# Kernel optimization log

Measured on AMD Instinct MI355X. Metric: run time of the kernel, lower is better.

## Reference

```python
import jax, jax.numpy as jnp
import numpy as np

N_HEAD = 16
G_HEADS = 2
D_HEAD = 64
D_MODEL = 1024
HEAD_RATIO = N_HEAD // G_HEADS  # 8
QK_DIM = G_HEADS * D_HEAD       # 128
SCALE = 1.0 / D_HEAD ** 0.5
LN_EPS = 1e-5


def _rel_shift(x):
    # x: [qlen, rlen, B, n] -- Transformer-XL relative shift
    q, r = x.shape[0], x.shape[1]
    x_pad = jnp.pad(x, ((0, 0), (1, 0), (0, 0), (0, 0)))      # [q, r+1, B, n]
    x_pad = x_pad.reshape(r + 1, q, *x.shape[2:])[1:]          # drop first row
    return x_pad.reshape(q, r, *x.shape[2:])


def setup_inputs() -> dict:
    key = jax.random.key(0)
    ks = jax.random.split(key, 9)
    qlen, bsz, levels = 1024, 4, 3
    w = jax.random.normal(ks[0], (qlen, bsz, D_MODEL), jnp.float32)
    r = jax.random.normal(ks[1], (qlen, D_MODEL), jnp.float32)
    r_w_bias = jax.random.normal(ks[2], (G_HEADS, D_HEAD), jnp.float32) * 0.02
    r_r_bias = jax.random.normal(ks[3], (G_HEADS, D_HEAD), jnp.float32) * 0.02
    masks = jax.random.uniform(ks[4], (qlen, qlen, levels), jnp.float32)
    W_qkv = jax.random.normal(ks[5], (2 * QK_DIM + N_HEAD * D_HEAD, D_MODEL), jnp.float32) * 0.02
    W_r = jax.random.normal(ks[6], (QK_DIM, D_MODEL), jnp.float32) * 0.02
    mask_proj = jnp.ones((levels, N_HEAD), jnp.float32)
    W_o = jax.random.normal(ks[7], (D_MODEL, N_HEAD * D_HEAD), jnp.float32) * 0.02
    ln_gamma = jnp.ones((D_MODEL,), jnp.float32)
    ln_beta = jnp.zeros((D_MODEL,), jnp.float32)
    return dict(w=w, r=r, r_w_bias=r_w_bias, r_r_bias=r_r_bias, masks=masks,
                W_qkv=W_qkv, W_r=W_r, mask_proj=mask_proj, W_o=W_o,
                ln_gamma=ln_gamma, ln_beta=ln_beta)


def reference(w, r, r_w_bias, r_r_bias, masks, W_qkv, W_r, mask_proj, W_o, ln_gamma, ln_beta):
    qlen, bsz, _ = w.shape
    rlen = r.shape[0]
    N = qlen  # no mems: klen == qlen == rlen

    w_heads = w @ W_qkv.T                                   # [q, B, 1280]
    r_head_k = (r @ W_r.T).reshape(rlen, G_HEADS, D_HEAD)   # [r, gH, d]
    w_head_q = w_heads[..., :QK_DIM].reshape(qlen, bsz, G_HEADS, D_HEAD)
    w_head_k = w_heads[..., QK_DIM:2 * QK_DIM].reshape(qlen, bsz, G_HEADS, D_HEAD)
    w_head_v = w_heads[..., 2 * QK_DIM:].reshape(qlen, bsz, N_HEAD, D_HEAD)

    AC = jnp.einsum('ibnd,jbnd->ijbn', w_head_q + r_w_bias, w_head_k)
    BD = jnp.einsum('ibnd,jnd->ijbn', w_head_q + r_r_bias, r_head_k)
    BD = _rel_shift(BD)
    attn_score = (AC + BD) * SCALE                           # [N, N, B, gH]

    # per-head mask mixing ('full' projection)
    attn = jnp.transpose(attn_score, (2, 3, 0, 1))           # [B, gH, N, N]
    mw = (masks @ mask_proj).reshape(N, N, G_HEADS, HEAD_RATIO)
    mw = jnp.transpose(mw, (2, 0, 1, 3))                     # [gH, N, N, hr]
    attn = attn[..., None] * mw[None]                        # [B, gH, N, N, hr]
    attn = jnp.transpose(attn, (0, 1, 4, 2, 3)).reshape(bsz, N_HEAD, N, N)
    attn_score = jnp.transpose(attn, (2, 3, 0, 1))           # [N, N, B, H]

    attn_prob = jax.nn.softmax(attn_score, axis=1)
    attn_vec = jnp.einsum('ijbn,jbnd->ibnd', attn_prob, w_head_v)
    attn_vec = attn_vec.reshape(qlen, bsz, N_HEAD * D_HEAD)
    attn_out = attn_vec @ W_o.T                              # [q, B, d_model]

    # post-LN residual
    x = w + attn_out
    mu = jnp.mean(x, axis=-1, keepdims=True)
    var = jnp.mean((x - mu) ** 2, axis=-1, keepdims=True)
    return (x - mu) * jax.lax.rsqrt(var + LN_EPS) * ln_gamma + ln_beta
```

## Files before the change

kernel.cpp:

```cpp
#include <hip/hip_runtime.h>
#include <cstddef>
#include <cstdint>

#define QLEN   1024
#define SCALE  0.125f
#define LN_EPS 1e-5f
#define DMODEL 1024

typedef __bf16 bf16x8 __attribute__((ext_vector_type(8)));
typedef __bf16 bf16x4 __attribute__((ext_vector_type(4)));
typedef float  f32x4  __attribute__((ext_vector_type(4)));

__device__ __forceinline__ void load16_lds(const void* g, void* l) {
  __builtin_amdgcn_global_load_lds(
      (const __attribute__((address_space(1))) unsigned int*)g,
      (__attribute__((address_space(3))) unsigned int*)l, 16, 0, 0);
}

__device__ __forceinline__ void bar_lds() {
  asm volatile("s_waitcnt lgkmcnt(0)" ::: "memory");
  __builtin_amdgcn_s_barrier();
  asm volatile("" ::: "memory");
}

__global__ __launch_bounds__(256) void cast_all(
    const float* __restrict__ w, __bf16* __restrict__ w_bf,
    const float* __restrict__ Wqkv, __bf16* __restrict__ Wqkv_bf,
    const float* __restrict__ r, __bf16* __restrict__ r_bf,
    const float* __restrict__ Wr, __bf16* __restrict__ Wr_bf,
    const float* __restrict__ Wo, __bf16* __restrict__ Wo_bf)
{
  int blk = blockIdx.x;
  const float* in; __bf16* out;
  if (blk < 2048)      { in = w;    out = w_bf;    }
  else if (blk < 2688) { blk -= 2048; in = Wqkv; out = Wqkv_bf; }
  else if (blk < 3200) { blk -= 2688; in = r;    out = r_bf;    }
  else if (blk < 3264) { blk -= 3200; in = Wr;   out = Wr_bf;   }
  else                 { blk -= 3264; in = Wo;   out = Wo_bf;   }
  const size_t i = ((size_t)blk * 256 + threadIdx.x) * 8;
  const float4 a = *(const float4*)&in[i];
  const float4 b = *(const float4*)&in[i + 4];
  bf16x8 o;
  o[0] = (__bf16)a.x; o[1] = (__bf16)a.y; o[2] = (__bf16)a.z; o[3] = (__bf16)a.w;
  o[4] = (__bf16)b.x; o[5] = (__bf16)b.y; o[6] = (__bf16)b.z; o[7] = (__bf16)b.w;
  *(bf16x8*)&out[i] = o;
}

__global__ __launch_bounds__(256) void gemm_proj(
    const __bf16* __restrict__ w_bf, const __bf16* __restrict__ Wqkv_bf,
    const __bf16* __restrict__ r_bf, const __bf16* __restrict__ Wr_bf,
    const float* __restrict__ rwb, const float* __restrict__ rrb,
    __bf16* __restrict__ Qw, __bf16* __restrict__ Qr,
    __bf16* __restrict__ Kb, __bf16* __restrict__ Vt,
    __bf16* __restrict__ Rb)
{
  __shared__ __bf16 Asl[128 * 32];
  __shared__ __bf16 Bsl[64 * 32];
  const int blk = blockIdx.x;
  const bool isR = blk >= 640;
  const __bf16 *A, *B;
  int m0, n0;
  if (!isR) { A = w_bf; B = Wqkv_bf; n0 = (blk % 20) * 64; m0 = (blk / 20) * 128; }
  else      { const int k = blk - 640; A = r_bf; B = Wr_bf;
              n0 = (k % 2) * 64; m0 = (k / 2) * 128; }

  const int tid = threadIdx.x, lane = tid & 63, wv = tid >> 6;
  const int lr = lane & 15, kq = lane >> 4;
  const int srow  = wv * 16 + (lane >> 2);
  const int sslot = lane & 3;
  const int sg0 = (sslot - ((srow >> 1) & 3)) & 3;
  const int sg1 = (sslot - (((srow + 64) >> 1) & 3)) & 3;
  const __bf16* Ag = A + (size_t)(m0 + srow) * 1024;
  const __bf16* Bg = B + (size_t)(n0 + srow) * 1024;
  __bf16* Al = &Asl[srow * 32 + sslot * 8];
  __bf16* Bl = &Bsl[srow * 32 + sslot * 8];

  f32x4 acc[2][4];
#pragma unroll
  for (int mt = 0; mt < 2; ++mt)
#pragma unroll
    for (int nt = 0; nt < 4; ++nt)
      acc[mt][nt] = (f32x4){0.f, 0.f, 0.f, 0.f};

  for (int k0 = 0; k0 < 1024; k0 += 32) {
    load16_lds(Ag + k0 + sg0 * 8, Al);
    load16_lds(Ag + (size_t)64 * 1024 + k0 + sg1 * 8, Al + 64 * 32);
    load16_lds(Bg + k0 + sg0 * 8, Bl);
    __syncthreads();
    bf16x8 af[2], bfr[4];
#pragma unroll
    for (int mt = 0; mt < 2; ++mt) {
      const int row = wv * 32 + mt * 16 + lr;
      af[mt] = *(const bf16x8*)&Asl[row * 32 + ((kq + (row >> 1)) & 3) * 8];
    }
#pragma unroll
    for (int nt = 0; nt < 4; ++nt) {
      const int row = nt * 16 + lr;
      bfr[nt] = *(const bf16x8*)&Bsl[row * 32 + ((kq + (row >> 1)) & 3) * 8];
    }
#pragma unroll
    for (int mt = 0; mt < 2; ++mt)
#pragma unroll
      for (int nt = 0; nt < 4; ++nt)
        acc[mt][nt] = __builtin_amdgcn_mfma_f32_16x16x32_bf16(
            af[mt], bfr[nt], acc[mt][nt], 0, 0, 0);
    __syncthreads();
  }

#pragma unroll
  for (int mt = 0; mt < 2; ++mt) {
    const int row0 = m0 + wv * 32 + mt * 16 + kq * 4;
#pragma unroll
    for (int nt = 0; nt < 4; ++nt) {
      const int gcol = n0 + nt * 16 + lr;
      const f32x4 c = acc[mt][nt];
      if (isR) {
        const int g = gcol >> 6, d = gcol & 63;
#pragma unroll
        for (int reg = 0; reg < 4; ++reg)
          Rb[(size_t)g * 65536 + (size_t)(row0 + reg) * 64 + d] = (__bf16)c[reg];
      } else if (gcol < 128) {
        const int g = gcol >> 6, d = gcol & 63;
        const float bw = rwb[gcol], br = rrb[gcol];
#pragma unroll
        for (int reg = 0; reg < 4; ++reg) {
          const int row = row0 + reg, i = row >> 2, b = row & 3;
          const size_t o = (size_t)(b * 2 + g) * 65536 + (size_t)i * 64 + d;
          Qw[o] = (__bf16)(c[reg] + bw);
          Qr[o] = (__bf16)(c[reg] + br);
        }
      } else if (gcol < 256) {
        const int lc = gcol - 128, g = lc >> 6, d = lc & 63;
#pragma unroll
        for (int reg = 0; reg < 4; ++reg) {
          const int row = row0 + reg, i = row >> 2, b = row & 3;
          Kb[(size_t)(b * 2 + g) * 65536 + (size_t)i * 64 + d] = (__bf16)c[reg];
        }
      } else {
        const int lc = gcol - 256, h = lc >> 6, d = lc & 63;
#pragma unroll
        for (int reg = 0; reg < 4; ++reg) {
          const int row = row0 + reg, i = row >> 2, b = row & 3;
          Vt[((size_t)((b * 16 + h) * 64 + d)) * 1024 + i] = (__bf16)c[reg];
        }
      }
    }
  }
}

__global__ __launch_bounds__(256) void gemm_wo(
    const __bf16* __restrict__ A, const __bf16* __restrict__ B,
    float* __restrict__ C)
{
  __shared__ __bf16 Asl[128 * 32];
  __shared__ __bf16 Bsl[64 * 32];
  const int m0 = blockIdx.y * 128, n0 = blockIdx.x * 64;
  const int tid = threadIdx.x, lane = tid & 63, wv = tid >> 6;
  const int lr = lane & 15, kq = lane >> 4;
  const int srow  = wv * 16 + (lane >> 2);
  const int sslot = lane & 3;
  const int sg0 = (sslot - ((srow >> 1) & 3)) & 3;
  const int sg1 = (sslot - (((srow + 64) >> 1) & 3)) & 3;
  const __bf16* Ag = A + (size_t)(m0 + srow) * 1024;
  const __bf16* Bg = B + (size_t)(n0 + srow) * 1024;
  __bf16* Al = &Asl[srow * 32 + sslot * 8];
  __bf16* Bl = &Bsl[srow * 32 + sslot * 8];

  f32x4 acc[2][4];
#pragma unroll
  for (int mt = 0; mt < 2; ++mt)
#pragma unroll
    for (int nt = 0; nt < 4; ++nt)
      acc[mt][nt] = (f32x4){0.f, 0.f, 0.f, 0.f};

  for (int k0 = 0; k0 < 1024; k0 += 32) {
    load16_lds(Ag + k0 + sg0 * 8, Al);
    load16_lds(Ag + (size_t)64 * 1024 + k0 + sg1 * 8, Al + 64 * 32);
    load16_lds(Bg + k0 + sg0 * 8, Bl);
    __syncthreads();
    bf16x8 af[2], bfr[4];
#pragma unroll
    for (int mt = 0; mt < 2; ++mt) {
      const int row = wv * 32 + mt * 16 + lr;
      af[mt] = *(const bf16x8*)&Asl[row * 32 + ((kq + (row >> 1)) & 3) * 8];
    }
#pragma unroll
    for (int nt = 0; nt < 4; ++nt) {
      const int row = nt * 16 + lr;
      bfr[nt] = *(const bf16x8*)&Bsl[row * 32 + ((kq + (row >> 1)) & 3) * 8];
    }
#pragma unroll
    for (int mt = 0; mt < 2; ++mt)
#pragma unroll
      for (int nt = 0; nt < 4; ++nt)
        acc[mt][nt] = __builtin_amdgcn_mfma_f32_16x16x32_bf16(
            af[mt], bfr[nt], acc[mt][nt], 0, 0, 0);
    __syncthreads();
  }

#pragma unroll
  for (int mt = 0; mt < 2; ++mt) {
    const int row0 = m0 + wv * 32 + mt * 16 + kq * 4;
#pragma unroll
    for (int nt = 0; nt < 4; ++nt) {
      const int col = n0 + nt * 16 + lr;
      const f32x4 c = acc[mt][nt];
#pragma unroll
      for (int reg = 0; reg < 4; ++reg)
        C[(size_t)(row0 + reg) * 1024 + col] = c[reg];
    }
  }
}

__global__ __launch_bounds__(256) void gemm64_bf16(
    const __bf16* __restrict__ Qw, const __bf16* __restrict__ Qr,
    const __bf16* __restrict__ Kb, const __bf16* __restrict__ Rb,
    __bf16* __restrict__ AC, __bf16* __restrict__ BDo)
{
  __shared__ __bf16 Asl[128 * 64];
  __shared__ __bf16 Bsl[128 * 64];
  const int tid = threadIdx.x, lane = tid & 63, wv = tid >> 6;
  const int which = blockIdx.z & 1, bat = blockIdx.z >> 1;
  const int m0 = blockIdx.y * 128, n0 = blockIdx.x * 128;
  const __bf16* Ap = (which ? Qr : Qw) + (size_t)bat * 65536;
  const __bf16* Bp = which ? (Rb + (size_t)(bat & 1) * 65536)
                           : (Kb + (size_t)bat * 65536);
  __bf16* Cp = (which ? BDo : AC) + (size_t)bat * 1048576;

#pragma unroll
  for (int p = 0; p < 4; ++p) {
    const int row = wv * 32 + p * 8 + (lane >> 3);
    const int s = lane & 7;
    const int gc = (s - (row & 7)) & 7;
    load16_lds(Ap + (size_t)(m0 + row) * 64 + gc * 8, &Asl[row * 64 + s * 8]);
    load16_lds(Bp + (size_t)(n0 + row) * 64 + gc * 8, &Bsl[row * 64 + s * 8]);
  }
  __syncthreads();

  const int lr = lane & 15, kq = lane >> 4;
  const int wm = (wv >> 1) * 64, wn = (wv & 1) * 64;
  f32x4 acc[4][4];
#pragma unroll
  for (int mt = 0; mt < 4; ++mt)
#pragma unroll
    for (int nt = 0; nt < 4; ++nt)
      acc[mt][nt] = (f32x4){0.f, 0.f, 0.f, 0.f};

#pragma unroll
  for (int ks = 0; ks < 2; ++ks) {
    const int c = ks * 4 + kq;
    bf16x8 af[4], bfr[4];
#pragma unroll
    for (int mt = 0; mt < 4; ++mt) {
      const int row = wm + mt * 16 + lr;
      af[mt] = *(const bf16x8*)&Asl[row * 64 + ((c + (row & 7)) & 7) * 8];
    }
#pragma unroll
    for (int nt = 0; nt < 4; ++nt) {
      const int row = wn + nt * 16 + lr;
      bfr[nt] = *(const bf16x8*)&Bsl[row * 64 + ((c + (row & 7)) & 7) * 8];
    }
#pragma unroll
    for (int mt = 0; mt < 4; ++mt)
#pragma unroll
      for (int nt = 0; nt < 4; ++nt)
        acc[mt][nt] = __builtin_amdgcn_mfma_f32_16x16x32_bf16(
            af[mt], bfr[nt], acc[mt][nt], 0, 0, 0);
  }

#pragma unroll
  for (int mt = 0; mt < 4; ++mt) {
    const int row0 = m0 + wm + mt * 16 + kq * 4;
#pragma unroll
    for (int nt = 0; nt < 4; ++nt) {
      const int col = n0 + wn + nt * 16 + lr;
      const f32x4 cc = acc[mt][nt];
#pragma unroll
      for (int reg = 0; reg < 4; ++reg)
        Cp[(size_t)(row0 + reg) * 1024 + col] = (__bf16)cc[reg];
    }
  }
}

__global__ __launch_bounds__(256) void prep2(
    const __bf16* __restrict__ AC, const __bf16* __restrict__ BDm,
    __bf16* __restrict__ Tg,
    const float* __restrict__ masks, const float* __restrict__ mproj,
    __bf16* __restrict__ Mh)
{
  const int tid = threadIdx.x;
  if (blockIdx.x < 2048) {
    const int blk = blockIdx.x;
    const size_t bg = blk >> 8;
    const int i = (blk & 255) * 4 + (tid >> 6);
    const int lane = tid & 63;
    const __bf16* ACr = AC + bg * 1048576 + (size_t)i * 1024;
    const __bf16* BDb = BDm + bg * 1048576;
    __bf16* Tr = Tg + bg * 1048576 + (size_t)i * 1024;
#pragma unroll
    for (int c2 = 0; c2 < 4; ++c2) {
      const int j0 = c2 * 256 + lane * 4;
      const bf16x4 ac4 = *(const bf16x4*)&ACr[j0];
      bf16x4 o;
#pragma unroll
      for (int k = 0; k < 4; ++k) {
        const int j = j0 + k;
        float bd;
        if (j <= i)          bd = (float)BDb[(size_t)i * 1024 + (j + QLEN - 1 - i)];
        else if (j == i + 1) bd = 0.f;
        else                 bd = (float)BDb[(size_t)(i + 1) * 1024 + (j - i - 2)];
        o[k] = (__bf16)(((float)ac4[k] + bd) * SCALE);
      }
      *(bf16x4*)&Tr[j0] = o;
    }
  } else {
    const int blk = blockIdx.x - 2048;
    const size_t ij0 = ((size_t)blk * 256 + tid) * 4;
    const float4 a = *(const float4*)&masks[ij0 * 3];
    const float4 b = *(const float4*)&masks[ij0 * 3 + 4];
    const float4 c = *(const float4*)&masks[ij0 * 3 + 8];
    const float m0[4] = {a.x, a.w, b.z, c.y};
    const float m1[4] = {a.y, b.x, b.w, c.z};
    const float m2[4] = {a.z, b.y, c.x, c.w};
#pragma unroll
    for (int h = 0; h < 16; ++h) {
      const float p0 = mproj[h], p1 = mproj[16 + h], p2 = mproj[32 + h];
      bf16x4 o;
#pragma unroll
      for (int k = 0; k < 4; ++k)
        o[k] = (__bf16)(m0[k] * p0 + m1[k] * p1 + m2[k] * p2);
      *(bf16x4*)&Mh[(size_t)h * 1048576 + ij0] = o;
    }
  }
}

__global__ __launch_bounds__(256, 4) void attn8(
    const __bf16* __restrict__ Tg, const __bf16* __restrict__ Mh,
    const __bf16* __restrict__ Vt, __bf16* __restrict__ av)
{
  __shared__ __bf16 P[2][32 * 256];
  __shared__ float rinvS[32];
  const int tid = threadIdx.x;
  const int i0 = blockIdx.x * 32;
  const int h = blockIdx.y, b = blockIdx.z;
  const int g = h >> 3;
  const size_t bg = (size_t)(b * 2 + g);
  const int r = tid >> 3, li = tid & 7;
  const __bf16* Trow = Tg + bg * 1048576 + (size_t)(i0 + r) * 1024 + li * 8;
  const __bf16* Mrow = Mh + (size_t)h * 1048576 + (size_t)(i0 + r) * 1024 + li * 8;

  const int lane = tid & 63, wv = tid >> 6;
  const int m = lane & 15, kq = lane >> 4;
  const __bf16* vbase = Vt + ((size_t)((b * 16 + h) * 64 + wv * 16 + m)) * 1024 + kq * 8;

  float sum = 0.f;
  f32x4 acc[2][2];
#pragma unroll
  for (int mt = 0; mt < 2; ++mt)
#pragma unroll
    for (int u = 0; u < 2; ++u)
      acc[mt][u] = (f32x4){0.f, 0.f, 0.f, 0.f};

  bf16x8 t[4], mk[4], v[8];
#pragma unroll
  for (int q = 0; q < 4; ++q) {
    t[q]  = *(const bf16x8*)&Trow[q * 64];
    mk[q] = *(const bf16x8*)&Mrow[q * 64];
  }

  for (int ch = 0; ch < 4; ++ch) {
    const int cb = ch & 1;
#pragma unroll
    for (int ks = 0; ks < 8; ++ks)
      v[ks] = *(const bf16x8*)&vbase[(ch * 8 + ks) * 32];
#pragma unroll
    for (int q = 0; q < 4; ++q) {
      bf16x8 p8;
      float s0 = 0.f;
#pragma unroll
      for (int k = 0; k < 8; ++k) {
        const float e = __expf((float)t[q][k] * (float)mk[q][k]);
        s0 += e;
        p8[k] = (__bf16)e;
      }
      sum += s0;
      const int slot = (q * 8 + li) ^ (r & 7);
      *(bf16x8*)&P[cb][r * 256 + slot * 8] = p8;
    }
    if (ch < 3) {
#pragma unroll
      for (int q = 0; q < 4; ++q) {
        t[q]  = *(const bf16x8*)&Trow[(ch + 1) * 256 + q * 64];
        mk[q] = *(const bf16x8*)&Mrow[(ch + 1) * 256 + q * 64];
      }
    }
    bar_lds();
#pragma unroll
    for (int ks = 0; ks < 8; ++ks) {
      const int c = ks * 4 + kq;
#pragma unroll
      for (int mt = 0; mt < 2; ++mt) {
        const int R = mt * 16 + m;
        const bf16x8 a = *(const bf16x8*)&P[cb][R * 256 + ((c ^ (R & 7)) << 3)];
        acc[mt][ks & 1] = __builtin_amdgcn_mfma_f32_16x16x32_bf16(
            a, v[ks], acc[mt][ks & 1], 0, 0, 0);
      }
    }
  }

  sum += __shfl_xor(sum, 1);
  sum += __shfl_xor(sum, 2);
  sum += __shfl_xor(sum, 4);
  if (li == 0) rinvS[r] = 1.f / sum;
  __syncthreads();

#pragma unroll
  for (int mt = 0; mt < 2; ++mt) {
    const f32x4 accf = acc[mt][0] + acc[mt][1];
#pragma unroll
    for (int reg = 0; reg < 4; ++reg) {
      const int row = mt * 16 + kq * 4 + reg;
      av[((size_t)(i0 + row) * 4 + b) * 1024 + h * 64 + wv * 16 + m] =
          (__bf16)(accf[reg] * rinvS[row]);
    }
  }
}

__global__ __launch_bounds__(256) void ln_kernel(
    const float* __restrict__ w, const float* __restrict__ ao,
    const float* __restrict__ gamma, const float* __restrict__ beta,
    float* __restrict__ out)
{
  const int tid = threadIdx.x;
  const size_t base = (size_t)blockIdx.x * DMODEL;
  __shared__ float red[256];
  float x[4];
  float s = 0.f;
#pragma unroll
  for (int p = 0; p < 4; ++p) {
    const int c = tid + p * 256;
    x[p] = w[base + c] + ao[base + c];
    s += x[p];
  }
  red[tid] = s; __syncthreads();
  for (int off = 128; off > 0; off >>= 1) {
    if (tid < off) red[tid] += red[tid + off];
    __syncthreads();
  }
  const float mu = red[0] * (1.f / DMODEL);
  __syncthreads();
  float s2 = 0.f;
#pragma unroll
  for (int p = 0; p < 4; ++p) { const float t = x[p] - mu; s2 += t * t; }
  red[tid] = s2; __syncthreads();
  for (int off = 128; off > 0; off >>= 1) {
    if (tid < off) red[tid] += red[tid + off];
    __syncthreads();
  }
  const float rs = rsqrtf(red[0] * (1.f / DMODEL) + LN_EPS);
#pragma unroll
  for (int p = 0; p < 4; ++p) {
    const int c = tid + p * 256;
    out[base + c] = (x[p] - mu) * rs * gamma[c] + beta[c];
  }
}

extern "C" void kernel_launch(void* const* d_in, const int* in_sizes, int n_in,
                              void* d_out, int out_size, void* d_ws, size_t ws_size,
                              hipStream_t stream)
{
  const float* w     = (const float*)d_in[0];
  const float* r     = (const float*)d_in[1];
  const float* rwb   = (const float*)d_in[2];
  const float* rrb   = (const float*)d_in[3];
  const float* masks = (const float*)d_in[4];
  const float* Wqkv  = (const float*)d_in[5];
  const float* Wr    = (const float*)d_in[6];
  const float* mproj = (const float*)d_in[7];
  const float* Wo    = (const float*)d_in[8];
  const float* gam   = (const float*)d_in[9];
  const float* bet   = (const float*)d_in[10];
  float* out = (float*)d_out;

  float* ws = (float*)d_ws;
  __bf16* w_bf    = (__bf16*)(ws);
  __bf16* Wqkv_bf = (__bf16*)(ws + 2097152);
  __bf16* r_bf    = (__bf16*)(ws + 2752512);
  __bf16* Wr_bf   = (__bf16*)(ws + 3276800);
  __bf16* Qw      = (__bf16*)(ws + 3342336);
  __bf16* Qr      = (__bf16*)(ws + 3604480);
  __bf16* Kb      = (__bf16*)(ws + 3866624);
  __bf16* Rb      = (__bf16*)(ws + 4128768);
  __bf16* Mh      = (__bf16*)(ws);
  __bf16* AC_bf   = (__bf16*)(ws + 8388608);
  float*  ao      = ws + 8388608;
  __bf16* BD_bf   = (__bf16*)(ws + 12582912);
  __bf16* Tg      = (__bf16*)(ws + 16777216);
  __bf16* Vt      = (__bf16*)(ws + 20971520);
  __bf16* av_bf   = (__bf16*)(ws + 23068672);
  __bf16* Wo_bf   = (__bf16*)(ws + 25165824);

  cast_all<<<3776, 256, 0, stream>>>(w, w_bf, Wqkv, Wqkv_bf, r, r_bf,
                                     Wr, Wr_bf, Wo, Wo_bf);
  gemm_proj<<<656, 256, 0, stream>>>(
      w_bf, Wqkv_bf, r_bf, Wr_bf, rwb, rrb, Qw, Qr, Kb, Vt, Rb);
  gemm64_bf16<<<dim3(8, 8, 16), 256, 0, stream>>>(Qw, Qr, Kb, Rb, AC_bf, BD_bf);
  prep2<<<3072, 256, 0, stream>>>(AC_bf, BD_bf, Tg, masks, mproj, Mh);
  attn8<<<dim3(32, 16, 4), 256, 0, stream>>>(Tg, Mh, Vt, av_bf);
  gemm_wo<<<dim3(16, 32), 256, 0, stream>>>(av_bf, Wo_bf, ao);
  ln_kernel<<<4096, 256, 0, stream>>>(w, ao, gam, bet, out);
}
```

Before: 237.1 us.

## Fuse rel-shift into BD GEMM store, merge score add into attention, enlarge GEMM tiles

The BD GEMM now writes its output directly in rel-shifted layout, and the attention kernel adds AC and shifted BD and applies the scale itself. This removes the prep2 pass that materialised the combined score tensor, leaving prep_mask to do only the mask projection. The projection and output GEMMs move from 128x64 to 128x128 tiles with a 2x2 wave layout, so each block reuses more data but there are fewer blocks and more registers per thread. The layer norm switches to float4 loads and wave-shuffle reductions. Attention now reads two score tensors instead of one, and the shifted store in the GEMM epilogue is scattered.

```diff
diff --git a/kernel.cpp b/kernel.cpp
--- a/kernel.cpp
+++ b/kernel.cpp
@@ -55,19 +55,18 @@
     __bf16* __restrict__ Rb)
 {
   __shared__ __bf16 Asl[128 * 32];
-  __shared__ __bf16 Bsl[64 * 32];
+  __shared__ __bf16 Bsl[128 * 32];
   const int blk = blockIdx.x;
-  const bool isR = blk >= 640;
+  const bool isR = blk >= 320;
   const __bf16 *A, *B;
   int m0, n0;
-  if (!isR) { A = w_bf; B = Wqkv_bf; n0 = (blk % 20) * 64; m0 = (blk / 20) * 128; }
-  else      { const int k = blk - 640; A = r_bf; B = Wr_bf;
-              n0 = (k % 2) * 64; m0 = (k / 2) * 128; }
+  if (!isR) { A = w_bf; B = Wqkv_bf; n0 = (blk % 10) * 128; m0 = (blk / 10) * 128; }
+  else      { A = r_bf; B = Wr_bf; n0 = 0; m0 = (blk - 320) * 128; }
 
   const int tid = threadIdx.x, lane = tid & 63, wv = tid >> 6;
   const int lr = lane & 15, kq = lane >> 4;
-  const int srow  = wv * 16 + (lane >> 2);
-  const int sslot = lane & 3;
+  const int srow  = tid >> 2;
+  const int sslot = tid & 3;
   const int sg0 = (sslot - ((srow >> 1) & 3)) & 3;
   const int sg1 = (sslot - (((srow + 64) >> 1) & 3)) & 3;
   const __bf16* Ag = A + (size_t)(m0 + srow) * 1024;
@@ -75,9 +74,11 @@
   __bf16* Al = &Asl[srow * 32 + sslot * 8];
   __bf16* Bl = &Bsl[srow * 32 + sslot * 8];
 
-  f32x4 acc[2][4];
-#pragma unroll
-  for (int mt = 0; mt < 2; ++mt)
+  const int mh = (wv >> 1) * 64, nh = (wv & 1) * 64;
+
+  f32x4 acc[4][4];
+#pragma unroll
+  for (int mt = 0; mt < 4; ++mt)
 #pragma unroll
     for (int nt = 0; nt < 4; ++nt)
       acc[mt][nt] = (f32x4){0.f, 0.f, 0.f, 0.f};
@@ -86,20 +87,21 @@
     load16_lds(Ag + k0 + sg0 * 8, Al);
     load16_lds(Ag + (size_t)64 * 1024 + k0 + sg1 * 8, Al + 64 * 32);
     load16_lds(Bg + k0 + sg0 * 8, Bl);
+    load16_lds(Bg + (size_t)64 * 1024 + k0 + sg1 * 8, Bl + 64 * 32);
     __syncthreads();
-    bf16x8 af[2], bfr[4];
-#pragma unroll
-    for (int mt = 0; mt < 2; ++mt) {
-      const int row = wv * 32 + mt * 16 + lr;
+    bf16x8 af[4], bfr[4];
+#pragma unroll
+    for (int mt = 0; mt < 4; ++mt) {
+      const int row = mh + mt * 16 + lr;
       af[mt] = *(const bf16x8*)&Asl[row * 32 + ((kq + (row >> 1)) & 3) * 8];
     }
 #pragma unroll
     for (int nt = 0; nt < 4; ++nt) {
-      const int row = nt * 16 + lr;
+      const int row = nh + nt * 16 + lr;
       bfr[nt] = *(const bf16x8*)&Bsl[row * 32 + ((kq + (row >> 1)) & 3) * 8];
     }
 #pragma unroll
-    for (int mt = 0; mt < 2; ++mt)
+    for (int mt = 0; mt < 4; ++mt)
 #pragma unroll
       for (int nt = 0; nt < 4; ++nt)
         acc[mt][nt] = __builtin_amdgcn_mfma_f32_16x16x32_bf16(
@@ -108,11 +110,11 @@
   }
 
 #pragma unroll
-  for (int mt = 0; mt < 2; ++mt) {
-    const int row0 = m0 + wv * 32 + mt * 16 + kq * 4;
+  for (int mt = 0; mt < 4; ++mt) {
+    const int row0 = m0 + mh + mt * 16 + kq * 4;
 #pragma unroll
     for (int nt = 0; nt < 4; ++nt) {
-      const int gcol = n0 + nt * 16 + lr;
+      const int gcol = n0 + nh + nt * 16 + lr;
       const f32x4 c = acc[mt][nt];
       if (isR) {
         const int g = gcol >> 6, d = gcol & 63;
@@ -153,12 +155,12 @@
     float* __restrict__ C)
 {
   __shared__ __bf16 Asl[128 * 32];
-  __shared__ __bf16 Bsl[64 * 32];
-  const int m0 = blockIdx.y * 128, n0 = blockIdx.x * 64;
+  __shared__ __bf16 Bsl[128 * 32];
+  const int m0 = blockIdx.y * 128, n0 = blockIdx.x * 128;
   const int tid = threadIdx.x, lane = tid & 63, wv = tid >> 6;
   const int lr = lane & 15, kq = lane >> 4;
-  const int srow  = wv * 16 + (lane >> 2);
-  const int sslot = lane & 3;
+  const int srow  = tid >> 2;
+  const int sslot = tid & 3;
   const int sg0 = (sslot - ((srow >> 1) & 3)) & 3;
   const int sg1 = (sslot - (((srow + 64) >> 1) & 3)) & 3;
   const __bf16* Ag = A + (size_t)(m0 + srow) * 1024;
@@ -166,9 +168,11 @@
   __bf16* Al = &Asl[srow * 32 + sslot * 8];
   __bf16* Bl = &Bsl[srow * 32 + sslot * 8];
 
-  f32x4 acc[2][4];
-#pragma unroll
-  for (int mt = 0; mt < 2; ++mt)
+  const int mh = (wv >> 1) * 64, nh = (wv & 1) * 64;
+
+  f32x4 acc[4][4];
+#pragma unroll
+  for (int mt = 0; mt < 4; ++mt)
 #pragma unroll
     for (int nt = 0; nt < 4; ++nt)
       acc[mt][nt] = (f32x4){0.f, 0.f, 0.f, 0.f};
@@ -177,20 +181,21 @@
     load16_lds(Ag + k0 + sg0 * 8, Al);
     load16_lds(Ag + (size_t)64 * 1024 + k0 + sg1 * 8, Al + 64 * 32);
     load16_lds(Bg + k0 + sg0 * 8, Bl);
+    load16_lds(Bg + (size_t)64 * 1024 + k0 + sg1 * 8, Bl + 64 * 32);
     __syncthreads();
-    bf16x8 af[2], bfr[4];
-#pragma unroll
-    for (int mt = 0; mt < 2; ++mt) {
-      const int row = wv * 32 + mt * 16 + lr;
+    bf16x8 af[4], bfr[4];
+#pragma unroll
+    for (int mt = 0; mt < 4; ++mt) {
+      const int row = mh + mt * 16 + lr;
       af[mt] = *(const bf16x8*)&Asl[row * 32 + ((kq + (row >> 1)) & 3) * 8];
     }
 #pragma unroll
     for (int nt = 0; nt < 4; ++nt) {
-      const int row = nt * 16 + lr;
+      const int row = nh + nt * 16 + lr;
       bfr[nt] = *(const bf16x8*)&Bsl[row * 32 + ((kq + (row >> 1)) & 3) * 8];
     }
 #pragma unroll
-    for (int mt = 0; mt < 2; ++mt)
+    for (int mt = 0; mt < 4; ++mt)
 #pragma unroll
       for (int nt = 0; nt < 4; ++nt)
         acc[mt][nt] = __builtin_amdgcn_mfma_f32_16x16x32_bf16(
@@ -199,11 +204,11 @@
   }
 
 #pragma unroll
-  for (int mt = 0; mt < 2; ++mt) {
-    const int row0 = m0 + wv * 32 + mt * 16 + kq * 4;
+  for (int mt = 0; mt < 4; ++mt) {
+    const int row0 = m0 + mh + mt * 16 + kq * 4;
 #pragma unroll
     for (int nt = 0; nt < 4; ++nt) {
-      const int col = n0 + nt * 16 + lr;
+      const int col = n0 + nh + nt * 16 + lr;
       const f32x4 c = acc[mt][nt];
 #pragma unroll
       for (int reg = 0; reg < 4; ++reg)
@@ -275,68 +280,54 @@
     for (int nt = 0; nt < 4; ++nt) {
       const int col = n0 + wn + nt * 16 + lr;
       const f32x4 cc = acc[mt][nt];
-#pragma unroll
-      for (int reg = 0; reg < 4; ++reg)
-        Cp[(size_t)(row0 + reg) * 1024 + col] = (__bf16)cc[reg];
-    }
-  }
-}
-
-__global__ __launch_bounds__(256) void prep2(
-    const __bf16* __restrict__ AC, const __bf16* __restrict__ BDm,
-    __bf16* __restrict__ Tg,
+      if (which) {
+#pragma unroll
+        for (int reg = 0; reg < 4; ++reg) {
+          const int k = row0 + reg;
+          const int thr = 1023 - k;
+          if (col >= thr) {
+            Cp[(size_t)k * 1024 + (col - thr)] = (__bf16)cc[reg];
+            if (col == thr && k < 1023)
+              Cp[(size_t)k * 1024 + (k + 1)] = (__bf16)0.f;
+          } else if (k > 0) {
+            Cp[(size_t)(k - 1) * 1024 + (col + k + 1)] = (__bf16)cc[reg];
+          }
+        }
+      } else {
+#pragma unroll
+        for (int reg = 0; reg < 4; ++reg)
+          Cp[(size_t)(row0 + reg) * 1024 + col] = (__bf16)cc[reg];
+      }
+    }
+  }
+}
+
+__global__ __launch_bounds__(256) void prep_mask(
     const float* __restrict__ masks, const float* __restrict__ mproj,
     __bf16* __restrict__ Mh)
 {
-  const int tid = threadIdx.x;
-  if (blockIdx.x < 2048) {
-    const int blk = blockIdx.x;
-    const size_t bg = blk >> 8;
-    const int i = (blk & 255) * 4 + (tid >> 6);
-    const int lane = tid & 63;
-    const __bf16* ACr = AC + bg * 1048576 + (size_t)i * 1024;
-    const __bf16* BDb = BDm + bg * 1048576;
-    __bf16* Tr = Tg + bg * 1048576 + (size_t)i * 1024;
-#pragma unroll
-    for (int c2 = 0; c2 < 4; ++c2) {
-      const int j0 = c2 * 256 + lane * 4;
-      const bf16x4 ac4 = *(const bf16x4*)&ACr[j0];
-      bf16x4 o;
-#pragma unroll
-      for (int k = 0; k < 4; ++k) {
-        const int j = j0 + k;
-        float bd;
-        if (j <= i)          bd = (float)BDb[(size_t)i * 1024 + (j + QLEN - 1 - i)];
-        else if (j == i + 1) bd = 0.f;
-        else                 bd = (float)BDb[(size_t)(i + 1) * 1024 + (j - i - 2)];
-        o[k] = (__bf16)(((float)ac4[k] + bd) * SCALE);
-      }
-      *(bf16x4*)&Tr[j0] = o;
-    }
-  } else {
-    const int blk = blockIdx.x - 2048;
-    const size_t ij0 = ((size_t)blk * 256 + tid) * 4;
-    const float4 a = *(const float4*)&masks[ij0 * 3];
-    const float4 b = *(const float4*)&masks[ij0 * 3 + 4];
-    const float4 c = *(const float4*)&masks[ij0 * 3 + 8];
-    const float m0[4] = {a.x, a.w, b.z, c.y};
-    const float m1[4] = {a.y, b.x, b.w, c.z};
-    const float m2[4] = {a.z, b.y, c.x, c.w};
-#pragma unroll
-    for (int h = 0; h < 16; ++h) {
-      const float p0 = mproj[h], p1 = mproj[16 + h], p2 = mproj[32 + h];
-      bf16x4 o;
-#pragma unroll
-      for (int k = 0; k < 4; ++k)
-        o[k] = (__bf16)(m0[k] * p0 + m1[k] * p1 + m2[k] * p2);
-      *(bf16x4*)&Mh[(size_t)h * 1048576 + ij0] = o;
-    }
-  }
-}
-
-__global__ __launch_bounds__(256, 4) void attn8(
-    const __bf16* __restrict__ Tg, const __bf16* __restrict__ Mh,
-    const __bf16* __restrict__ Vt, __bf16* __restrict__ av)
+  const size_t ij0 = ((size_t)blockIdx.x * 256 + threadIdx.x) * 4;
+  const float4 a = *(const float4*)&masks[ij0 * 3];
+  const float4 b = *(const float4*)&masks[ij0 * 3 + 4];
+  const float4 c = *(const float4*)&masks[ij0 * 3 + 8];
+  const float m0[4] = {a.x, a.w, b.z, c.y};
+  const float m1[4] = {a.y, b.x, b.w, c.z};
+  const float m2[4] = {a.z, b.y, c.x, c.w};
+#pragma unroll
+  for (int h = 0; h < 16; ++h) {
+    const float p0 = mproj[h], p1 = mproj[16 + h], p2 = mproj[32 + h];
+    bf16x4 o;
+#pragma unroll
+    for (int k = 0; k < 4; ++k)
+      o[k] = (__bf16)(m0[k] * p0 + m1[k] * p1 + m2[k] * p2);
+    *(bf16x4*)&Mh[(size_t)h * 1048576 + ij0] = o;
+  }
+}
+
+__global__ __launch_bounds__(256, 4) void attn9(
+    const __bf16* __restrict__ ACb, const __bf16* __restrict__ BDs,
+    const __bf16* __restrict__ Mh, const __bf16* __restrict__ Vt,
+    __bf16* __restrict__ av)
 {
   __shared__ __bf16 P[2][32 * 256];
   __shared__ float rinvS[32];
@@ -346,8 +337,9 @@
   const int g = h >> 3;
   const size_t bg = (size_t)(b * 2 + g);
   const int r = tid >> 3, li = tid & 7;
-  const __bf16* Trow = Tg + bg * 1048576 + (size_t)(i0 + r) * 1024 + li * 8;
-  const __bf16* Mrow = Mh + (size_t)h * 1048576 + (size_t)(i0 + r) * 1024 + li * 8;
+  const __bf16* ACrow = ACb + bg * 1048576 + (size_t)(i0 + r) * 1024 + li * 8;
+  const __bf16* BDrow = BDs + bg * 1048576 + (size_t)(i0 + r) * 1024 + li * 8;
+  const __bf16* Mrow  = Mh + (size_t)h * 1048576 + (size_t)(i0 + r) * 1024 + li * 8;
 
   const int lane = tid & 63, wv = tid >> 6;
   const int m = lane & 15, kq = lane >> 4;
@@ -361,10 +353,11 @@
     for (int u = 0; u < 2; ++u)
       acc[mt][u] = (f32x4){0.f, 0.f, 0.f, 0.f};
 
-  bf16x8 t[4], mk[4], v[8];
+  bf16x8 ac[4], bd[4], mk[4], v[8];
 #pragma unroll
   for (int q = 0; q < 4; ++q) {
-    t[q]  = *(const bf16x8*)&Trow[q * 64];
+    ac[q] = *(const bf16x8*)&ACrow[q * 64];
+    bd[q] = *(const bf16x8*)&BDrow[q * 64];
     mk[q] = *(const bf16x8*)&Mrow[q * 64];
   }
 
@@ -379,7 +372,8 @@
       float s0 = 0.f;
 #pragma unroll
       for (int k = 0; k < 8; ++k) {
-        const float e = __expf((float)t[q][k] * (float)mk[q][k]);
+        const float t = ((float)ac[q][k] + (float)bd[q][k]) * SCALE;
+        const float e = __expf(t * (float)mk[q][k]);
         s0 += e;
         p8[k] = (__bf16)e;
       }
@@ -390,7 +384,8 @@
     if (ch < 3) {
 #pragma unroll
       for (int q = 0; q < 4; ++q) {
-        t[q]  = *(const bf16x8*)&Trow[(ch + 1) * 256 + q * 64];
+        ac[q] = *(const bf16x8*)&ACrow[(ch + 1) * 256 + q * 64];
+        bd[q] = *(const bf16x8*)&BDrow[(ch + 1) * 256 + q * 64];
         mk[q] = *(const bf16x8*)&Mrow[(ch + 1) * 256 + q * 64];
       }
     }
@@ -432,37 +427,34 @@
     float* __restrict__ out)
 {
   const int tid = threadIdx.x;
-  const size_t base = (size_t)blockIdx.x * DMODEL;
-  __shared__ float red[256];
-  float x[4];
-  float s = 0.f;
-#pragma unroll
-  for (int p = 0; p < 4; ++p) {
-    const int c = tid + p * 256;
-    x[p] = w[base + c] + ao[base + c];
-    s += x[p];
-  }
-  red[tid] = s; __syncthreads();
-  for (int off = 128; off > 0; off >>= 1) {
-    if (tid < off) red[tid] += red[tid + off];
-    __syncthreads();
-  }
-  const float mu = red[0] * (1.f / DMODEL);
+  const int lane = tid & 63, wv = tid >> 6;
+  const size_t base = (size_t)blockIdx.x * DMODEL + tid * 4;
+  __shared__ float red[8];
+  const float4 xw = *(const float4*)&w[base];
+  const float4 xa = *(const float4*)&ao[base];
+  float x[4] = {xw.x + xa.x, xw.y + xa.y, xw.z + xa.z, xw.w + xa.w};
+  float s = (x[0] + x[1]) + (x[2] + x[3]);
+  s += __shfl_xor(s, 1);  s += __shfl_xor(s, 2);  s += __shfl_xor(s, 4);
+  s += __shfl_xor(s, 8);  s += __shfl_xor(s, 16); s += __shfl_xor(s, 32);
+  if (lane == 0) red[wv] = s;
   __syncthreads();
+  const float mu = (red[0] + red[1] + red[2] + red[3]) * (1.f / DMODEL);
   float s2 = 0.f;
 #pragma unroll
   for (int p = 0; p < 4; ++p) { const float t = x[p] - mu; s2 += t * t; }
-  red[tid] = s2; __syncthreads();
-  for (int off = 128; off > 0; off >>= 1) {
-    if (tid < off) red[tid] += red[tid + off];
-    __syncthreads();
-  }
-  const float rs = rsqrtf(red[0] * (1.f / DMODEL) + LN_EPS);
-#pragma unroll
-  for (int p = 0; p < 4; ++p) {
-    const int c = tid + p * 256;
-    out[base + c] = (x[p] - mu) * rs * gamma[c] + beta[c];
-  }
+  s2 += __shfl_xor(s2, 1);  s2 += __shfl_xor(s2, 2);  s2 += __shfl_xor(s2, 4);
+  s2 += __shfl_xor(s2, 8);  s2 += __shfl_xor(s2, 16); s2 += __shfl_xor(s2, 32);
+  if (lane == 0) red[4 + wv] = s2;
+  __syncthreads();
+  const float rs = rsqrtf((red[4] + red[5] + red[6] + red[7]) * (1.f / DMODEL) + LN_EPS);
+  const float4 g4 = *(const float4*)&gamma[tid * 4];
+  const float4 b4 = *(const float4*)&beta[tid * 4];
+  float4 o;
+  o.x = (x[0] - mu) * rs * g4.x + b4.x;
+  o.y = (x[1] - mu) * rs * g4.y + b4.y;
+  o.z = (x[2] - mu) * rs * g4.z + b4.z;
+  o.w = (x[3] - mu) * rs * g4.w + b4.w;
+  *(float4*)&out[base] = o;
 }
 
 extern "C" void kernel_launch(void* const* d_in, const int* in_sizes, int n_in,
@@ -495,18 +487,17 @@
   __bf16* AC_bf   = (__bf16*)(ws + 8388608);
   float*  ao      = ws + 8388608;
   __bf16* BD_bf   = (__bf16*)(ws + 12582912);
-  __bf16* Tg      = (__bf16*)(ws + 16777216);
   __bf16* Vt      = (__bf16*)(ws + 20971520);
   __bf16* av_bf   = (__bf16*)(ws + 23068672);
   __bf16* Wo_bf   = (__bf16*)(ws + 25165824);
 
   cast_all<<<3776, 256, 0, stream>>>(w, w_bf, Wqkv, Wqkv_bf, r, r_bf,
                                      Wr, Wr_bf, Wo, Wo_bf);
-  gemm_proj<<<656, 256, 0, stream>>>(
+  gemm_proj<<<328, 256, 0, stream>>>(
       w_bf, Wqkv_bf, r_bf, Wr_bf, rwb, rrb, Qw, Qr, Kb, Vt, Rb);
   gemm64_bf16<<<dim3(8, 8, 16), 256, 0, stream>>>(Qw, Qr, Kb, Rb, AC_bf, BD_bf);
-  prep2<<<3072, 256, 0, stream>>>(AC_bf, BD_bf, Tg, masks, mproj, Mh);
-  attn8<<<dim3(32, 16, 4), 256, 0, stream>>>(Tg, Mh, Vt, av_bf);
-  gemm_wo<<<dim3(16, 32), 256, 0, stream>>>(av_bf, Wo_bf, ao);
+  prep_mask<<<1024, 256, 0, stream>>>(masks, mproj, Mh);
+  attn9<<<dim3(32, 16, 4), 256, 0, stream>>>(AC_bf, BD_bf, Mh, Vt, av_bf);
+  gemm_wo<<<dim3(8, 32), 256, 0, stream>>>(av_bf, Wo_bf, ao);
   ln_kernel<<<4096, 256, 0, stream>>>(w, ao, gam, bet, out);
 }
```

Result: slower. 247.7 us (+4.5%).
